# Optimization experiments

Measured on AMD Instinct MI355X. Metric: run time of the kernel, lower is better.

Reference implementation:

```python
import jax, jax.numpy as jnp
import numpy as np

B, N, EMBED, CHEB_K, INP, HID = 32, 8192, 16, 2, 2, 64


def setup_inputs() -> dict:
    key = jax.random.key(0)
    k1, k2, k3, k4 = jax.random.split(key, 4)
    return {
        "x": jax.random.normal(k1, (B, N, INP), dtype=jnp.float32),
        "adj": jax.random.normal(k2, (N, EMBED), dtype=jnp.float32),
        "weights_pool": jax.random.normal(k3, (EMBED, CHEB_K, INP, HID), dtype=jnp.float32) * 0.1,
        "bias_pool": jax.random.normal(k4, (EMBED, HID), dtype=jnp.float32) * 0.1,
    }


def reference(x, adj, weights_pool, bias_pool):
    n = adj.shape[0]
    cheb_k = weights_pool.shape[1]
    # adaptive adjacency: row-softmax of relu(E E^T)
    ADJ = jax.nn.softmax(jax.nn.relu(adj @ adj.T), axis=1)  # [n, n]
    support_set = [jnp.eye(n, dtype=x.dtype), ADJ]
    for k in range(2, cheb_k):  # Chebyshev recursion (fixed small k)
        support_set.append(2.0 * ADJ @ support_set[-1] - support_set[-2])
    supports = jnp.stack(support_set, axis=0)  # [k, n, n]
    # node-adaptive weights / bias
    weights = jnp.einsum("nd,dkio->nkio", adj, weights_pool)  # [n,k,inp,hid]
    bias = adj @ bias_pool  # [n, hid]
    # graph propagation, directly in bnkc layout (fuses the permute)
    x_g = jnp.einsum("knm,bmc->bnkc", supports, x)  # [b,n,k,inp]
    out = jnp.einsum("bnki,nkio->bno", x_g, weights) + bias  # [b,n,hid]
    return out
```

## Files before the change

### kernel.cpp

```cpp
#include <hip/hip_runtime.h>

#define NN 8192
#define BB 32
#define EMB 16
#define HID 64
#define MS 16
#define TM 64

typedef __attribute__((ext_vector_type(8))) short bf16x8;
typedef __attribute__((ext_vector_type(4))) float f32x4;

static __device__ inline unsigned short f2b(float f) {
    union { float f; unsigned u; } v; v.f = f;
    return (unsigned short)((v.u + 0x7fffu + ((v.u >> 16) & 1u)) >> 16);
}

__global__ void k_build(const float* __restrict__ x, const float* __restrict__ adj,
                        const float* __restrict__ wp, const float* __restrict__ bp,
                        short* __restrict__ VTf, short* __restrict__ Afrag,
                        short* __restrict__ adjS, float* __restrict__ Wbuf) {
    const int t = threadIdx.x;
    const int bx = blockIdx.x;
    if (bx < 256) {
        const int c = bx;
        const int u = t >> 6, lane = t & 63, l = lane & 15, q = lane >> 4;
        const int j = 16 * u + l, b = j >> 1, ch = j & 1;
        const int m0 = 32 * c + 8 * q;
        const float* xp = x + (size_t)b * (NN * 2) + m0 * 2;
        uint4 d;
        unsigned dd[4];
#pragma unroll
        for (int i = 0; i < 4; ++i) {
            float4 xx = *(const float4*)(xp + 4 * i);
            float v0 = ch ? xx.y : xx.x;
            float v1 = ch ? xx.w : xx.z;
            dd[i] = (unsigned)f2b(v0) | ((unsigned)f2b(v1) << 16);
        }
        d.x = dd[0]; d.y = dd[1]; d.z = dd[2]; d.w = dd[3];
        *(uint4*)(VTf + ((size_t)(c * 4 + u) * 64 + lane) * 8) = d;
    } else if (bx < 384) {
        const int cc = t >> 7, tt = t & 127;
        const int c = (bx - 256) * 2 + cc;
        const int h = tt >> 6, lane = tt & 63, l = lane & 15, q = lane >> 4;
        const int row = 32 * c + 8 * (l >> 2) + (l & 3) + 4 * h;
        const float* ap = adj + (size_t)row * EMB + (q & 1) * 8;
        float4 a0 = *(const float4*)(ap);
        float4 a1 = *(const float4*)(ap + 4);
        uint4 d;
        d.x = (unsigned)f2b(a0.x) | ((unsigned)f2b(a0.y) << 16);
        d.y = (unsigned)f2b(a0.z) | ((unsigned)f2b(a0.w) << 16);
        d.z = (unsigned)f2b(a1.x) | ((unsigned)f2b(a1.y) << 16);
        d.w = (unsigned)f2b(a1.z) | ((unsigned)f2b(a1.w) << 16);
        *(uint4*)(Afrag + ((size_t)(c * 2 + h) * 64 + lane) * 8) = d;
    } else if (bx < 512) {
        const float L2E = 1.4426950408889634f;
        int idx = (bx - 384) * 256 + t;
        float4 aa = *(const float4*)(adj + (size_t)idx * 4);
        uint2 us;
        us.x = (unsigned)f2b(aa.x * L2E) | ((unsigned)f2b(aa.y * L2E) << 16);
        us.y = (unsigned)f2b(aa.z * L2E) | ((unsigned)f2b(aa.w * L2E) << 16);
        *(uint2*)(adjS + (size_t)idx * 4) = us;
    } else {
        const int nl = t >> 4, og = t & 15;
        const int n = (bx - 512) * 16 + nl;
        const float4* wp4 = (const float4*)wp;
        const float4* bp4 = (const float4*)bp;
        float an[EMB];
#pragma unroll
        for (int d = 0; d < EMB; ++d) an[d] = adj[n * EMB + d];
        float4 w[5];
#pragma unroll
        for (int c = 0; c < 5; ++c) { w[c].x = w[c].y = w[c].z = w[c].w = 0.f; }
#pragma unroll
        for (int d = 0; d < EMB; ++d) {
            float a = an[d];
#pragma unroll
            for (int c = 0; c < 4; ++c) {
                float4 p = wp4[(d * 4 + c) * 16 + og];
                w[c].x += a * p.x; w[c].y += a * p.y; w[c].z += a * p.z; w[c].w += a * p.w;
            }
            float4 pb = bp4[d * 16 + og];
            w[4].x += a * pb.x; w[4].y += a * pb.y; w[4].z += a * pb.z; w[4].w += a * pb.w;
        }
#pragma unroll
        for (int c = 0; c < 5; ++c)
            *(float4*)(Wbuf + (size_t)n * 320 + c * 64 + og * 4) = w[c];
    }
}

__launch_bounds__(256, 4)
__global__ void k_prop(const short* __restrict__ Afrag, const short* __restrict__ adjS,
                       const short* __restrict__ VTf,
                       short* __restrict__ ynum, float* __restrict__ den) {
    const int t = threadIdx.x;
    const int wv = t >> 6;
    const int lane = t & 63;
    const int l = lane & 15;
    const int q = lane >> 4;
    const int n0 = blockIdx.x * 128 + wv * 32;
    const int cbeg = blockIdx.y * (NN / MS / 32);
    const int cend = cbeg + (NN / MS / 32);

    bf16x8 Bn[2];
    bf16x8 zv = {0, 0, 0, 0, 0, 0, 0, 0};
#pragma unroll
    for (int s = 0; s < 2; ++s) {
        const short* src = adjS + (size_t)(n0 + 16 * s + l) * EMB + (q & 1) * 8;
        bf16x8 v = *(const bf16x8*)src;
        Bn[s] = (q < 2) ? v : zv;
    }
    const short one = (short)0x3F80;
    bf16x8 ones = {one, one, one, one, one, one, one, one};

    f32x4 acc[4][2];
    f32x4 dacc[2];
#pragma unroll
    for (int u = 0; u < 4; ++u)
#pragma unroll
        for (int s = 0; s < 2; ++s) { acc[u][s][0] = acc[u][s][1] = acc[u][s][2] = acc[u][s][3] = 0.f; }
#pragma unroll
    for (int s = 0; s < 2; ++s) { dacc[s][0] = dacc[s][1] = dacc[s][2] = dacc[s][3] = 0.f; }

    for (int cg = cbeg; cg < cend; ++cg) {
        bf16x8 Af0 = *(const bf16x8*)(Afrag + ((size_t)(cg * 2 + 0) * 64 + lane) * 8);
        bf16x8 Af1 = *(const bf16x8*)(Afrag + ((size_t)(cg * 2 + 1) * 64 + lane) * 8);
        bf16x8 Vf[4];
#pragma unroll
        for (int u = 0; u < 4; ++u)
            Vf[u] = *(const bf16x8*)(VTf + ((size_t)(cg * 4 + u) * 64 + lane) * 8);

        f32x4 z = {0.f, 0.f, 0.f, 0.f};
        f32x4 S0[2], S1[2];
#pragma unroll
        for (int s = 0; s < 2; ++s) {
            S0[s] = __builtin_amdgcn_mfma_f32_16x16x32_bf16(Af0, Bn[s], z, 0, 0, 0);
            S1[s] = __builtin_amdgcn_mfma_f32_16x16x32_bf16(Af1, Bn[s], z, 0, 0, 0);
        }
#pragma unroll
        for (int s = 0; s < 2; ++s) {
            unsigned wb[8];
#pragma unroll
            for (int r = 0; r < 4; ++r) {
                union { float f; unsigned u; } p0, p1;
                p0.f = __builtin_amdgcn_exp2f(fmaxf(S0[s][r], 0.f));
                p1.f = __builtin_amdgcn_exp2f(fmaxf(S1[s][r], 0.f));
                wb[r] = p0.u;
                wb[4 + r] = p1.u;
            }
            union { bf16x8 v; unsigned d[4]; } pf;
#pragma unroll
            for (int dd = 0; dd < 4; ++dd)
                pf.d[dd] = (wb[2 * dd + 1] & 0xFFFF0000u) | (wb[2 * dd] >> 16);
#pragma unroll
            for (int u = 0; u < 4; ++u)
                acc[u][s] = __builtin_amdgcn_mfma_f32_16x16x32_bf16(Vf[u], pf.v, acc[u][s], 0, 0, 0);
            dacc[s] = __builtin_amdgcn_mfma_f32_16x16x32_bf16(ones, pf.v, dacc[s], 0, 0, 0);
        }
    }

    short* yp = ynum + (size_t)blockIdx.y * NN * HID;
#pragma unroll
    for (int s = 0; s < 2; ++s) {
        const int n = n0 + 16 * s + l;
#pragma unroll
        for (int u = 0; u < 4; ++u) {
            union { float f; unsigned u; } a0, a1, a2, a3;
            a0.f = acc[u][s][0]; a1.f = acc[u][s][1]; a2.f = acc[u][s][2]; a3.f = acc[u][s][3];
            uint2 pk;
            pk.x = (a1.u & 0xFFFF0000u) | (a0.u >> 16);
            pk.y = (a3.u & 0xFFFF0000u) | (a2.u >> 16);
            *(uint2*)(yp + (size_t)n * HID + 16 * u + 4 * q) = pk;
        }
        if (q == 0) den[(size_t)blockIdx.y * NN + n] = dacc[s][0];
    }
}

__global__ void k_epi(const float* __restrict__ Wbuf, const float* __restrict__ x,
                      const short* __restrict__ ynum, const float* __restrict__ den,
                      float* __restrict__ out) {
    const int nl = threadIdx.x >> 4, og = threadIdx.x & 15;
    const int n = blockIdx.x * 16 + nl;
    __shared__ float xl[16][68];
    __shared__ float yl[16][68];

    float4 W[5];
#pragma unroll
    for (int c = 0; c < 5; ++c)
        W[c] = *(const float4*)(Wbuf + (size_t)n * 320 + c * 64 + og * 4);

    float4 ysum; ysum.x = ysum.y = ysum.z = ysum.w = 0.f;
    float dsum = 0.f;
#pragma unroll
    for (int s = 0; s < MS; ++s) {
        ushort4 p = *(const ushort4*)(ynum + ((size_t)s * NN + n) * HID + og * 4);
        union { unsigned u; float f; } c0, c1, c2, c3;
        c0.u = (unsigned)p.x << 16; c1.u = (unsigned)p.y << 16;
        c2.u = (unsigned)p.z << 16; c3.u = (unsigned)p.w << 16;
        ysum.x += c0.f; ysum.y += c1.f; ysum.z += c2.f; ysum.w += c3.f;
        dsum += den[(size_t)s * NN + n];
    }
    float rden = 1.f / dsum;
    *(float4*)&yl[nl][og * 4] = make_float4(ysum.x * rden, ysum.y * rden, ysum.z * rden, ysum.w * rden);

    float2 x0 = *(const float2*)(x + ((size_t)(og * 2) * NN + n) * 2);
    float2 x1 = *(const float2*)(x + ((size_t)(og * 2 + 1) * NN + n) * 2);
    xl[nl][og * 4 + 0] = x0.x; xl[nl][og * 4 + 1] = x0.y;
    xl[nl][og * 4 + 2] = x1.x; xl[nl][og * 4 + 3] = x1.y;
    __syncthreads();

#pragma unroll 4
    for (int b = 0; b < BB; ++b) {
        float xb0 = xl[nl][2 * b], xb1 = xl[nl][2 * b + 1];
        float yb0 = yl[nl][2 * b], yb1 = yl[nl][2 * b + 1];
        float4 o4;
        o4.x = xb0 * W[0].x + xb1 * W[1].x + yb0 * W[2].x + yb1 * W[3].x + W[4].x;
        o4.y = xb0 * W[0].y + xb1 * W[1].y + yb0 * W[2].y + yb1 * W[3].y + W[4].y;
        o4.z = xb0 * W[0].z + xb1 * W[1].z + yb0 * W[2].z + yb1 * W[3].z + W[4].z;
        o4.w = xb0 * W[0].w + xb1 * W[1].w + yb0 * W[2].w + yb1 * W[3].w + W[4].w;
        *(float4*)(out + ((size_t)b * NN + n) * HID + og * 4) = o4;
    }
}

extern "C" void kernel_launch(void* const* d_in, const int* in_sizes, int n_in,
                              void* d_out, int out_size, void* d_ws, size_t ws_size,
                              hipStream_t stream) {
    const float* x   = (const float*)d_in[0];
    const float* adj = (const float*)d_in[1];
    const float* wp  = (const float*)d_in[2];
    const float* bp  = (const float*)d_in[3];
    float* out = (float*)d_out;

    char* w = (char*)d_ws;
    short* VTf   = (short*)w;
    short* Afrag = VTf + (size_t)256 * 4 * 64 * 8;
    short* adjS  = Afrag + (size_t)256 * 2 * 64 * 8;
    float* Wbuf  = (float*)(adjS + (size_t)NN * EMB);
    short* ynum  = (short*)(Wbuf + (size_t)NN * 320);
    float* den   = (float*)(ynum + (size_t)MS * NN * HID);

    k_build<<<1024, 256, 0, stream>>>(x, adj, wp, bp, VTf, Afrag, adjS, Wbuf);
    k_prop<<<dim3(NN / 128, MS), 256, 0, stream>>>(Afrag, adjS, VTf, ynum, den);
    k_epi<<<NN / 16, 256, 0, stream>>>(Wbuf, x, ynum, den, out);
}
```

Baseline: 133.0 us.

## Double-buffer prop loads, store node weights as bf16, use perm packing and nontemporal stores

The propagation loop now software-pipelines fragment loads with a two-stage double buffer, and launch bounds drop from 4 to 3 blocks per SM to make room for the extra registers. Per-node weights are stored in bf16 instead of fp32, which halves Wbuf traffic between build and epilogue at some cost in precision. bf16 packing uses a byte-permute builtin. Output stores in the epilogue are nontemporal to avoid cache pollution.

```diff
diff --git a/kernel.cpp b/kernel.cpp
--- a/kernel.cpp
+++ b/kernel.cpp
@@ -5,7 +5,6 @@
 #define EMB 16
 #define HID 64
 #define MS 16
-#define TM 64
 
 typedef __attribute__((ext_vector_type(8))) short bf16x8;
 typedef __attribute__((ext_vector_type(4))) float f32x4;
@@ -15,10 +14,18 @@
     return (unsigned short)((v.u + 0x7fffu + ((v.u >> 16) & 1u)) >> 16);
 }
 
+static __device__ inline unsigned packbf(unsigned e_even, unsigned e_odd) {
+#if __has_builtin(__builtin_amdgcn_perm)
+    return __builtin_amdgcn_perm(e_odd, e_even, 0x07060302u);
+#else
+    return (e_odd & 0xFFFF0000u) | (e_even >> 16);
+#endif
+}
+
 __global__ void k_build(const float* __restrict__ x, const float* __restrict__ adj,
                         const float* __restrict__ wp, const float* __restrict__ bp,
                         short* __restrict__ VTf, short* __restrict__ Afrag,
-                        short* __restrict__ adjS, float* __restrict__ Wbuf) {
+                        short* __restrict__ adjS, unsigned short* __restrict__ WbufB) {
     const int t = threadIdx.x;
     const int bx = blockIdx.x;
     if (bx < 256) {
@@ -83,12 +90,15 @@
             w[4].x += a * pb.x; w[4].y += a * pb.y; w[4].z += a * pb.z; w[4].w += a * pb.w;
         }
 #pragma unroll
-        for (int c = 0; c < 5; ++c)
-            *(float4*)(Wbuf + (size_t)n * 320 + c * 64 + og * 4) = w[c];
-    }
-}
-
-__launch_bounds__(256, 4)
+        for (int c = 0; c < 5; ++c) {
+            ushort4 pk;
+            pk.x = f2b(w[c].x); pk.y = f2b(w[c].y); pk.z = f2b(w[c].z); pk.w = f2b(w[c].w);
+            *(ushort4*)(WbufB + (size_t)n * 320 + c * 64 + og * 4) = pk;
+        }
+    }
+}
+
+__launch_bounds__(256, 3)
 __global__ void k_prop(const short* __restrict__ Afrag, const short* __restrict__ adjS,
                        const short* __restrict__ VTf,
                        short* __restrict__ ynum, float* __restrict__ den) {
@@ -121,14 +131,20 @@
 #pragma unroll
     for (int s = 0; s < 2; ++s) { dacc[s][0] = dacc[s][1] = dacc[s][2] = dacc[s][3] = 0.f; }
 
-    for (int cg = cbeg; cg < cend; ++cg) {
-        bf16x8 Af0 = *(const bf16x8*)(Afrag + ((size_t)(cg * 2 + 0) * 64 + lane) * 8);
-        bf16x8 Af1 = *(const bf16x8*)(Afrag + ((size_t)(cg * 2 + 1) * 64 + lane) * 8);
-        bf16x8 Vf[4];
-#pragma unroll
-        for (int u = 0; u < 4; ++u)
-            Vf[u] = *(const bf16x8*)(VTf + ((size_t)(cg * 4 + u) * 64 + lane) * 8);
-
+    const short* Ap = Afrag + (size_t)lane * 8;
+    const short* Vp = VTf + (size_t)lane * 8;
+
+#define LOADF(cg, a0, a1, vv)                                            \
+    do {                                                                 \
+        a0 = *(const bf16x8*)(Ap + (size_t)(cg) * 1024);                 \
+        a1 = *(const bf16x8*)(Ap + (size_t)(cg) * 1024 + 512);           \
+        vv[0] = *(const bf16x8*)(Vp + (size_t)(cg) * 2048);              \
+        vv[1] = *(const bf16x8*)(Vp + (size_t)(cg) * 2048 + 512);        \
+        vv[2] = *(const bf16x8*)(Vp + (size_t)(cg) * 2048 + 1024);       \
+        vv[3] = *(const bf16x8*)(Vp + (size_t)(cg) * 2048 + 1536);       \
+    } while (0)
+
+    auto compute = [&](bf16x8 Af0, bf16x8 Af1, bf16x8* Vf) {
         f32x4 z = {0.f, 0.f, 0.f, 0.f};
         f32x4 S0[2], S1[2];
 #pragma unroll
@@ -138,25 +154,37 @@
         }
 #pragma unroll
         for (int s = 0; s < 2; ++s) {
-            unsigned wb[8];
+            unsigned w0[4], w1[4];
 #pragma unroll
             for (int r = 0; r < 4; ++r) {
                 union { float f; unsigned u; } p0, p1;
                 p0.f = __builtin_amdgcn_exp2f(fmaxf(S0[s][r], 0.f));
                 p1.f = __builtin_amdgcn_exp2f(fmaxf(S1[s][r], 0.f));
-                wb[r] = p0.u;
-                wb[4 + r] = p1.u;
+                w0[r] = p0.u;
+                w1[r] = p1.u;
             }
             union { bf16x8 v; unsigned d[4]; } pf;
-#pragma unroll
-            for (int dd = 0; dd < 4; ++dd)
-                pf.d[dd] = (wb[2 * dd + 1] & 0xFFFF0000u) | (wb[2 * dd] >> 16);
+            pf.d[0] = packbf(w0[0], w0[1]);
+            pf.d[1] = packbf(w0[2], w0[3]);
+            pf.d[2] = packbf(w1[0], w1[1]);
+            pf.d[3] = packbf(w1[2], w1[3]);
 #pragma unroll
             for (int u = 0; u < 4; ++u)
                 acc[u][s] = __builtin_amdgcn_mfma_f32_16x16x32_bf16(Vf[u], pf.v, acc[u][s], 0, 0, 0);
             dacc[s] = __builtin_amdgcn_mfma_f32_16x16x32_bf16(ones, pf.v, dacc[s], 0, 0, 0);
         }
-    }
+    };
+
+    bf16x8 a0A, a1A, vA[4], a0B, a1B, vB[4];
+    LOADF(cbeg, a0A, a1A, vA);
+    for (int cg = cbeg; cg < cend; cg += 2) {
+        LOADF(cg + 1, a0B, a1B, vB);
+        compute(a0A, a1A, vA);
+        int cg2 = (cg + 2 < cend) ? cg + 2 : cbeg;
+        LOADF(cg2, a0A, a1A, vA);
+        compute(a0B, a1B, vB);
+    }
+#undef LOADF
 
     short* yp = ynum + (size_t)blockIdx.y * NN * HID;
 #pragma unroll
@@ -167,15 +195,15 @@
             union { float f; unsigned u; } a0, a1, a2, a3;
             a0.f = acc[u][s][0]; a1.f = acc[u][s][1]; a2.f = acc[u][s][2]; a3.f = acc[u][s][3];
             uint2 pk;
-            pk.x = (a1.u & 0xFFFF0000u) | (a0.u >> 16);
-            pk.y = (a3.u & 0xFFFF0000u) | (a2.u >> 16);
+            pk.x = packbf(a0.u, a1.u);
+            pk.y = packbf(a2.u, a3.u);
             *(uint2*)(yp + (size_t)n * HID + 16 * u + 4 * q) = pk;
         }
         if (q == 0) den[(size_t)blockIdx.y * NN + n] = dacc[s][0];
     }
 }
 
-__global__ void k_epi(const float* __restrict__ Wbuf, const float* __restrict__ x,
+__global__ void k_epi(const unsigned short* __restrict__ WbufB, const float* __restrict__ x,
                       const short* __restrict__ ynum, const float* __restrict__ den,
                       float* __restrict__ out) {
     const int nl = threadIdx.x >> 4, og = threadIdx.x & 15;
@@ -185,8 +213,13 @@
 
     float4 W[5];
 #pragma unroll
-    for (int c = 0; c < 5; ++c)
-        W[c] = *(const float4*)(Wbuf + (size_t)n * 320 + c * 64 + og * 4);
+    for (int c = 0; c < 5; ++c) {
+        ushort4 pw = *(const ushort4*)(WbufB + (size_t)n * 320 + c * 64 + og * 4);
+        union { unsigned u; float f; } c0, c1, c2, c3;
+        c0.u = (unsigned)pw.x << 16; c1.u = (unsigned)pw.y << 16;
+        c2.u = (unsigned)pw.z << 16; c3.u = (unsigned)pw.w << 16;
+        W[c].x = c0.f; W[c].y = c1.f; W[c].z = c2.f; W[c].w = c3.f;
+    }
 
     float4 ysum; ysum.x = ysum.y = ysum.z = ysum.w = 0.f;
     float dsum = 0.f;
@@ -212,12 +245,12 @@
     for (int b = 0; b < BB; ++b) {
         float xb0 = xl[nl][2 * b], xb1 = xl[nl][2 * b + 1];
         float yb0 = yl[nl][2 * b], yb1 = yl[nl][2 * b + 1];
-        float4 o4;
-        o4.x = xb0 * W[0].x + xb1 * W[1].x + yb0 * W[2].x + yb1 * W[3].x + W[4].x;
-        o4.y = xb0 * W[0].y + xb1 * W[1].y + yb0 * W[2].y + yb1 * W[3].y + W[4].y;
-        o4.z = xb0 * W[0].z + xb1 * W[1].z + yb0 * W[2].z + yb1 * W[3].z + W[4].z;
-        o4.w = xb0 * W[0].w + xb1 * W[1].w + yb0 * W[2].w + yb1 * W[3].w + W[4].w;
-        *(float4*)(out + ((size_t)b * NN + n) * HID + og * 4) = o4;
+        f32x4 o4;
+        o4[0] = xb0 * W[0].x + xb1 * W[1].x + yb0 * W[2].x + yb1 * W[3].x + W[4].x;
+        o4[1] = xb0 * W[0].y + xb1 * W[1].y + yb0 * W[2].y + yb1 * W[3].y + W[4].y;
+        o4[2] = xb0 * W[0].z + xb1 * W[1].z + yb0 * W[2].z + yb1 * W[3].z + W[4].z;
+        o4[3] = xb0 * W[0].w + xb1 * W[1].w + yb0 * W[2].w + yb1 * W[3].w + W[4].w;
+        __builtin_nontemporal_store(o4, (f32x4*)(out + ((size_t)b * NN + n) * HID + og * 4));
     }
 }
 
@@ -234,11 +267,11 @@
     short* VTf   = (short*)w;
     short* Afrag = VTf + (size_t)256 * 4 * 64 * 8;
     short* adjS  = Afrag + (size_t)256 * 2 * 64 * 8;
-    float* Wbuf  = (float*)(adjS + (size_t)NN * EMB);
-    short* ynum  = (short*)(Wbuf + (size_t)NN * 320);
+    unsigned short* WbufB = (unsigned short*)(adjS + (size_t)NN * EMB);
+    short* ynum  = (short*)(WbufB + (size_t)NN * 320);
     float* den   = (float*)(ynum + (size_t)MS * NN * HID);
 
-    k_build<<<1024, 256, 0, stream>>>(x, adj, wp, bp, VTf, Afrag, adjS, Wbuf);
+    k_build<<<1024, 256, 0, stream>>>(x, adj, wp, bp, VTf, Afrag, adjS, WbufB);
     k_prop<<<dim3(NN / 128, MS), 256, 0, stream>>>(Afrag, adjS, VTf, ynum, den);
-    k_epi<<<NN / 16, 256, 0, stream>>>(Wbuf, x, ynum, den, out);
-}
+    k_epi<<<NN / 16, 256, 0, stream>>>(WbufB, x, ynum, den, out);
+}
```

New measurement: 121.9 us. -8.4%, faster.
